# Kernel optimization log

Measured on AMD Instinct MI355X. Metric: run time of the kernel, lower is better.

## Reference

```python
import jax, jax.numpy as jnp
import numpy as np

IMAGE_SIZE = 1280
STRIDES = (8, 16, 32)
NUM_CLASSES = 80
BPC = 3  # boxes per cell
NMS_THRESH = 0.5
CONF_THRESH = 0.3
K_LEVEL = 1000
K_TOTAL = 3 * K_LEVEL
CLASS_OFFSET = 1.0e7  # shift boxes per class so cross-class IoU == 0 (== per-class NMS)
ANCHORS = np.array([[10,13],[16,30],[33,23],[30,61],[62,45],[59,119],
                    [116,90],[156,198],[373,326]], np.float32).reshape(3, 3, 2)

def level_anchors(level):
    f = IMAGE_SIZE // STRIDES[level]
    gy, gx = jnp.meshgrid(jnp.arange(f), jnp.arange(f), indexing='ij')
    xy = jnp.stack([gx, gy], -1).astype(jnp.float32).reshape(f * f, 1, 2)
    xy = jnp.broadcast_to(xy, (f * f, BPC, 2)).reshape(-1, 2)
    wh = jnp.broadcast_to(jnp.asarray(ANCHORS[level]), (f * f, BPC, 2)).reshape(-1, 2)
    return jnp.concatenate([xy, wh], -1)  # [M, 4]

def decode_boxes(anchors, reg, level):
    ctr = (jax.nn.sigmoid(reg[:, :2]) + anchors[:, :2]) * STRIDES[level]
    wh = jnp.exp(reg[:, 2:]) * anchors[:, 2:]
    return jnp.concatenate([ctr - wh * 0.5, ctr + wh * 0.5], -1)  # [M, 4] x1y1x2y2

def topk_level(obj, cls, reg, level):
    boxes = decode_boxes(level_anchors(level), reg, level)          # [M, 4]
    scores = jnp.sqrt(jax.nn.sigmoid(obj) * jax.nn.sigmoid(cls))    # [M, C]
    top_s, top_i = jax.lax.top_k(scores.reshape(-1), K_LEVEL)       # over M*C
    anchor_idx = top_i // NUM_CLASSES
    labels = top_i % NUM_CLASSES
    return top_s, labels, boxes[anchor_idx]

def nms_keep(boxes, scores, labels, valid):
    # Replicate source nms(): decoded x1y1x2y2 boxes are (re-)treated as cxcywh.
    b = jnp.concatenate([boxes[:, :2] - boxes[:, 2:] * 0.5,
                         boxes[:, :2] + boxes[:, 2:] * 0.5], -1)
    # class-aware: offset x-coords per class label
    off = labels.astype(jnp.float32) * CLASS_OFFSET
    b = b + off[:, None] * jnp.array([1.0, 0.0, 1.0, 0.0], b.dtype)
    x1, y1, x2, y2 = b[:, 0], b[:, 1], b[:, 2], b[:, 3]
    area = (x2 - x1) * (y2 - y1)
    xx1 = jnp.maximum(x1[:, None], x1[None, :])
    yy1 = jnp.maximum(y1[:, None], y1[None, :])
    xx2 = jnp.minimum(x2[:, None], x2[None, :])
    yy2 = jnp.minimum(y2[:, None], y2[None, :])
    inter = jnp.maximum(1e-10, xx2 - xx1) * jnp.maximum(1e-10, yy2 - yy1)
    iou = inter / (area[:, None] + area[None, :] - inter + 1e-14)   # [K, K]
    idx = jnp.arange(boxes.shape[0])
    def body(i, keep):
        sup = (iou[i] > NMS_THRESH) & (idx > i) & keep[i]
        return keep & ~sup
    return jax.lax.fori_loop(0, boxes.shape[0], body, valid)

def setup_inputs():
    key = jax.random.key(0)
    ks = jax.random.split(key, 9)
    d = {}
    for lvl, M in enumerate([76800, 19200, 4800]):
        d[f'obj{lvl}'] = jax.random.normal(ks[3 * lvl + 0], (M, 1), jnp.float32)
        d[f'cls{lvl}'] = jax.random.normal(ks[3 * lvl + 1], (M, NUM_CLASSES), jnp.float32)
        d[f'reg{lvl}'] = jax.random.normal(ks[3 * lvl + 2], (M, 4), jnp.float32)
    return d

def reference(obj0, cls0, reg0, obj1, cls1, reg1, obj2, cls2, reg2):
    levels = [(obj0, cls0, reg0), (obj1, cls1, reg1), (obj2, cls2, reg2)]
    ss, ls, bs = zip(*[topk_level(o, c, r, lvl) for lvl, (o, c, r) in enumerate(levels)])
    scores = jnp.concatenate(ss)        # [K_TOTAL]
    labels = jnp.concatenate(ls)
    boxes = jnp.concatenate(bs)         # [K_TOTAL, 4]
    # global sort by score (descending) so greedy NMS visits in score order
    scores, order = jax.lax.top_k(scores, K_TOTAL)
    labels = labels[order]
    boxes = boxes[order]
    valid = scores > CONF_THRESH
    keep = nms_keep(boxes, scores, labels, valid)
    out_boxes = jnp.where(keep[:, None], boxes, 0.0)
    out_scores = jnp.where(keep, scores, 0.0)
    out_labels = jnp.where(keep, labels, -1).astype(jnp.int32)
    return out_boxes, out_scores, out_labels, keep
```

## Files before the change

kernel.cpp:

```cpp
#include <hip/hip_runtime.h>
#include <hip/hip_bf16.h>
#include <math.h>

typedef unsigned int u32;
typedef unsigned long long u64;

#define NCLS 80
#define KLVL 1000
#define CAP  8192
#define TARGET_S 160u

#define OFF_CAND   0u
#define OFF_HIST   196608u
#define OFF_CNT    221184u
#define OFF_GFLAT  221216u
#define OFF_GSB    233216u
#define OFF_QX1    245216u
#define OFF_QY1    257216u
#define OFF_QX2    269216u
#define OFF_QY2    281216u
#define OFF_AREA   293216u
#define OFF_SCORE  305216u
#define OFF_LABEL  317216u
#define OFF_VALID  329216u
#define OFF_OBOX   341216u

__constant__ float cANCH[3][3][2] = {
  {{10.f,13.f},{16.f,30.f},{33.f,23.f}},
  {{30.f,61.f},{62.f,45.f},{59.f,119.f}},
  {{116.f,90.f},{156.f,198.f},{373.f,326.f}}
};

__device__ __forceinline__ float sig_fast(float x) {
  return 1.0f / (1.0f + __expf(-x));
}
__device__ __forceinline__ float sig_crit(float x) {
#pragma clang fp contract(off)
  double e = exp(-(double)x);
  float ef = (float)e;
  return 1.0f / (1.0f + ef);
}

__global__ __launch_bounds__(256) void kA(u32* __restrict__ hist,
                                          u32* __restrict__ cnt,
                                          u32* __restrict__ gsbits,
                                          u32* __restrict__ gflat) {
  int t = blockIdx.x * 256 + threadIdx.x;
  if (t < 6144) hist[t] = 0u;
  else if (t < 6152) cnt[t - 6144] = 0u;
  else if (t < 9152) gsbits[t - 6152] = 0u;
  else if (t < 12152) gflat[t - 9152] = 0u;
}

__global__ __launch_bounds__(256) void kB_s(const float* __restrict__ c0,
                                            const float* __restrict__ c1,
                                            const float* __restrict__ c2,
                                            const float* __restrict__ o0,
                                            const float* __restrict__ o1,
                                            const float* __restrict__ o2,
                                            u32* __restrict__ ghist) {
  __shared__ u32 lh[2048];
  for (int i = threadIdx.x; i < 2048; i += 256) lh[i] = 0u;
  __syncthreads();
  int bid = blockIdx.x;
  int l, e0; const float* cls; const float* obj;
  if (bid < 375)      { l = 0; e0 = (bid * 16 + 8) * 1024;         cls = c0; obj = o0; }
  else if (bid < 469) { l = 1; e0 = ((bid - 375) * 16 + 8) * 1024; cls = c1; obj = o1; }
  else                { l = 2; e0 = ((bid - 469) * 16 + 8) * 1024; cls = c2; obj = o2; }
  int e = e0 + threadIdx.x * 4;
  float4 cv = *(const float4*)(cls + e);
  float so = sig_fast(obj[e / 80]);
  float cc[4] = {cv.x, cv.y, cv.z, cv.w};
#pragma unroll
  for (int k = 0; k < 4; k++) {
    float p = so * sig_fast(cc[k]);
    atomicAdd(&lh[__float_as_uint(p) >> 19], 1u);
  }
  __syncthreads();
  for (int i = threadIdx.x; i < 2048; i += 256) {
    u32 v = lh[i];
    if (v) atomicAdd(&ghist[l * 2048 + i], v);
  }
}

__global__ __launch_bounds__(64) void k2(const u32* __restrict__ ghist,
                                         u32* __restrict__ cnt) {
  int l = blockIdx.x;
  int lane = threadIdx.x;
  const u32* h = ghist + l * 2048;
  int top = 2047 - lane * 32;
  u32 s = 0;
#pragma unroll
  for (int i = 0; i < 32; i++) s += h[top - i];
  u32 pre = s;
#pragma unroll
  for (int off = 1; off < 64; off <<= 1) {
    u32 o = __shfl_up(pre, off);
    if (lane >= off) pre += o;
  }
  u64 m = __ballot(pre >= TARGET_S);
  if (m == 0ull) { if (lane == 0) cnt[4 + l] = 0u; return; }
  int sel = __ffsll((long long)m) - 1;
  if (lane == sel) {
    u32 c = pre - s;
    u32 bb = 0u;
    for (int i = 0; i < 32; i++) {
      c += h[top - i];
      if (c >= TARGET_S) { bb = (u32)(top - i); break; }
    }
    cnt[4 + l] = bb << 19;
  }
}

__device__ __forceinline__ void block_map(int bid, int& l, int& e0) {
  if (bid < 6000)      { l = 0; e0 = bid * 1024; }
  else if (bid < 7500) { l = 1; e0 = (bid - 6000) * 1024; }
  else                 { l = 2; e0 = (bid - 7500) * 1024; }
}

__global__ __launch_bounds__(256) void k3(const float* __restrict__ c0,
                                          const float* __restrict__ c1,
                                          const float* __restrict__ c2,
                                          const float* __restrict__ o0,
                                          const float* __restrict__ o1,
                                          const float* __restrict__ o2,
                                          u32* __restrict__ cnt,
                                          u64* __restrict__ cand) {
  int l, e0; block_map(blockIdx.x, l, e0);
  const float* cls = (l == 0) ? c0 : (l == 1) ? c1 : c2;
  const float* obj = (l == 0) ? o0 : (l == 1) ? o1 : o2;
  u32 T = cnt[4 + l];
  u32 Tm = (T > 64u) ? (T - 64u) : 0u;
  int e = e0 + threadIdx.x * 4;
  float4 cv = *(const float4*)(cls + e);
  int a = e / 80;
  float so = sig_fast(obj[a]);
  float cc[4] = {cv.x, cv.y, cv.z, cv.w};
#pragma unroll
  for (int k = 0; k < 4; k++) {
    float pch = so * sig_fast(cc[k]);
    if (__float_as_uint(pch) >= Tm) {
      float soe = sig_crit(obj[a]);
      float sce = sig_crit(cc[k]);
      float p = soe * sce;
      u32 bits = __float_as_uint(p);
      if (bits >= T) {
        u32 slot = atomicAdd(&cnt[l], 1u);
        if (slot < CAP) {
          float s = __fsqrt_rn(p);
          u64 key = ((u64)__float_as_uint(s) << 32) | (u32)(~((u32)(e + k)));
          cand[(size_t)l * CAP + slot] = key;
        }
      }
    }
  }
}

__global__ __launch_bounds__(64) void r1(const u64* __restrict__ cand,
                                         const u32* __restrict__ cnt,
                                         u32* __restrict__ gsbits,
                                         u32* __restrict__ gflat) {
  __shared__ u64 S[CAP];
  int l = blockIdx.x >> 7;
  int b = blockIdx.x & 127;
  u32 n = cnt[l]; if (n > CAP) n = CAP;
  if ((u32)(b * 64) >= n) return;
  const u64* base = cand + (size_t)l * CAP;
  for (u32 i = threadIdx.x; i < n; i += 64) S[i] = base[i];
  __syncthreads();
  u32 idx = (u32)(b * 64 + threadIdx.x);
  u64 my = (idx < n) ? S[idx] : 0ull;
  u32 rank = 0;
#pragma unroll 8
  for (u32 i = 0; i < n; ++i) rank += (S[i] > my) ? 1u : 0u;
  if (idx < n && rank < KLVL) {
    gsbits[l * KLVL + rank] = (u32)(my >> 32);
    gflat [l * KLVL + rank] = ~((u32)my);
  }
}

__global__ __launch_bounds__(64) void rk6(const float* __restrict__ r0,
                                          const float* __restrict__ r1_,
                                          const float* __restrict__ r2_,
                                          const u32* __restrict__ gsbits,
                                          const u32* __restrict__ gflat,
                                          float* __restrict__ qx1, float* __restrict__ qy1,
                                          float* __restrict__ qx2, float* __restrict__ qy2,
                                          float* __restrict__ area,
                                          float* __restrict__ score,
                                          u32* __restrict__ label,
                                          u32* __restrict__ valid,
                                          float* __restrict__ obox,
                                          float* __restrict__ out) {
#pragma clang fp contract(off)
  __shared__ u32 SB[3000];
  int t = blockIdx.x * 64 + threadIdx.x;
  for (u32 i = threadIdx.x; i < 3000; i += 64) SB[i] = gsbits[i];
  __syncthreads();
  if (t >= 3000) return;
  ((float4*)out)[t] = make_float4(0.f, 0.f, 0.f, 0.f);
  out[12000 + t] = 0.0f;
  out[15000 + t] = -1.0f;
  out[18000 + t] = 0.0f;
  u32 myb = SB[t];
  u64 my = (((u64)myb) << 32) | (u32)(~t);
  u32 rank = 0;
#pragma unroll 8
  for (int i = 0; i < 3000; ++i) {
    u64 k = (((u64)SB[i]) << 32) | (u32)(~i);
    rank += (k > my) ? 1u : 0u;
  }
  int l = t / 1000;
  u32 flat = gflat[t];
  float sc = __uint_as_float(myb);
  int a = (int)(flat / NCLS), c = (int)(flat % NCLS);
  int cell = a / 3, bi = a % 3;
  int f = (l == 0) ? 160 : (l == 1) ? 80 : 40;
  float stride = (float)(8 << l);
  float gx = (float)(cell % f), gy = (float)(cell / f);
  const float* rp = ((l == 0) ? r0 : (l == 1) ? r1_ : r2_) + (size_t)a * 4;
  float t0 = rp[0], t1 = rp[1], t2 = rp[2], t3 = rp[3];
  float sx = 1.0f / (1.0f + expf(-t0));
  float sy = 1.0f / (1.0f + expf(-t1));
  float w = expf(t2) * cANCH[l][bi][0];
  float h = expf(t3) * cANCH[l][bi][1];
  float cx = (sx + gx) * stride;
  float cy = (sy + gy) * stride;
  float hw = w * 0.5f, hh = h * 0.5f;
  float x1 = cx - hw, y1 = cy - hh, x2 = cx + hw, y2 = cy + hh;
  ((float4*)obox)[rank] = make_float4(x1, y1, x2, y2);
  float hx2 = x2 * 0.5f, hy2 = y2 * 0.5f;
  float bx1 = x1 - hx2, by1 = y1 - hy2, bx2 = x1 + hx2, by2 = y1 + hy2;
  float off = (float)c * 1e7f;
  float a1 = bx1 + off, a2 = bx2 + off;
  qx1[rank] = a1; qy1[rank] = by1; qx2[rank] = a2; qy2[rank] = by2;
  area[rank] = (a2 - a1) * (by2 - by1);
  score[rank] = sc; label[rank] = (u32)c;
  valid[rank] = (sc > 0.3f) ? 1u : 0u;
}

#define CAPC 1024
__global__ __launch_bounds__(64) void k7(const float* __restrict__ qx1,
                                         const float* __restrict__ qy1,
                                         const float* __restrict__ qx2,
                                         const float* __restrict__ qy2,
                                         const float* __restrict__ area,
                                         const float* __restrict__ score,
                                         const u32* __restrict__ label,
                                         const u32* __restrict__ valid,
                                         const float* __restrict__ obox,
                                         float* __restrict__ out) {
#pragma clang fp contract(off)
  __shared__ u32 LIST[CAPC];
  __shared__ float X1[CAPC], Y1[CAPC], X2[CAPC], Y2[CAPC], AR[CAPC];
  __shared__ u32 KP[CAPC];
  u32 c = blockIdx.x;
  int lane = threadIdx.x;
  u32 n = 0;
  for (int base = 0; base < 3000; base += 64) {
    int j = base + lane;
    bool m = false;
    if (j < 3000) m = (label[j] == c) && (valid[j] != 0u);
    u64 mask = __ballot(m ? 1 : 0);
    u32 pos = n + (u32)__popcll(mask & ((1ull << lane) - 1ull));
    if (m && pos < CAPC) {
      LIST[pos] = (u32)j;
      X1[pos] = qx1[j]; Y1[pos] = qy1[j];
      X2[pos] = qx2[j]; Y2[pos] = qy2[j];
      AR[pos] = area[j]; KP[pos] = 1u;
    }
    n += (u32)__popcll(mask);
  }
  if (n > CAPC) n = CAPC;
  __syncthreads();
  for (u32 i = 0; i < n; ++i) {
    if (KP[i]) {
      float xi1 = X1[i], yi1 = Y1[i], xi2 = X2[i], yi2 = Y2[i], ai = AR[i];
      for (u32 j = i + 1 + (u32)lane; j < n; j += 64) {
        if (KP[j]) {
          float xx1 = fmaxf(xi1, X1[j]);
          float yy1 = fmaxf(yi1, Y1[j]);
          float xx2 = fminf(xi2, X2[j]);
          float yy2 = fminf(yi2, Y2[j]);
          float iw = xx2 - xx1, ih = yy2 - yy1;
          float inter = fmaxf(1e-10f, iw) * fmaxf(1e-10f, ih);
          float den = ai + AR[j] - inter + 1e-14f;
          if (inter / den > 0.5f) KP[j] = 0u;
        }
      }
    }
    __syncthreads();
  }
  for (u32 j = (u32)lane; j < n; j += 64) {
    if (KP[j]) {
      u32 r = LIST[j];
      float4 bx = ((const float4*)obox)[r];
      ((float4*)out)[r] = bx;
      out[12000 + r] = score[r];
      out[15000 + r] = (float)(int)c;
      out[18000 + r] = 1.0f;
    }
  }
}

extern "C" void kernel_launch(void* const* d_in, const int* in_sizes, int n_in,
                              void* d_out, int out_size, void* d_ws, size_t ws_size,
                              hipStream_t stream) {
  const float* obj0 = (const float*)d_in[0];
  const float* cls0 = (const float*)d_in[1];
  const float* reg0 = (const float*)d_in[2];
  const float* obj1 = (const float*)d_in[3];
  const float* cls1 = (const float*)d_in[4];
  const float* reg1 = (const float*)d_in[5];
  const float* obj2 = (const float*)d_in[6];
  const float* cls2 = (const float*)d_in[7];
  const float* reg2 = (const float*)d_in[8];
  char* ws = (char*)d_ws;
  u64* cand   = (u64*)(ws + OFF_CAND);
  u32* hist   = (u32*)(ws + OFF_HIST);
  u32* cnt    = (u32*)(ws + OFF_CNT);
  u32* gflat  = (u32*)(ws + OFF_GFLAT);
  u32* gsbits = (u32*)(ws + OFF_GSB);
  float* qx1  = (float*)(ws + OFF_QX1);
  float* qy1  = (float*)(ws + OFF_QY1);
  float* qx2  = (float*)(ws + OFF_QX2);
  float* qy2  = (float*)(ws + OFF_QY2);
  float* area = (float*)(ws + OFF_AREA);
  float* score= (float*)(ws + OFF_SCORE);
  u32* label  = (u32*)(ws + OFF_LABEL);
  u32* valid  = (u32*)(ws + OFF_VALID);
  float* obox = (float*)(ws + OFF_OBOX);
  float* out  = (float*)d_out;

  kA<<<48, 256, 0, stream>>>(hist, cnt, gsbits, gflat);
  kB_s<<<492, 256, 0, stream>>>(cls0, cls1, cls2, obj0, obj1, obj2, hist);
  k2<<<3, 64, 0, stream>>>(hist, cnt);
  k3<<<7875, 256, 0, stream>>>(cls0, cls1, cls2, obj0, obj1, obj2, cnt, cand);
  r1<<<384, 64, 0, stream>>>(cand, cnt, gsbits, gflat);
  rk6<<<47, 64, 0, stream>>>(reg0, reg1, reg2, gsbits, gflat,
                             qx1, qy1, qx2, qy2, area, score, label, valid, obox, out);
  k7<<<80, 64, 0, stream>>>(qx1, qy1, qx2, qy2, area, score, label, valid, obox, out);
}
```

Baseline: 332.1 us.

## Precompute per-anchor logit thresholds and filter 16-class chunks by max

Adds a small kernel that converts each anchor's objectness and the level threshold into a minimum class logit, so the candidate scan can reject classes by a raw compare instead of evaluating a sigmoid per element. The candidate kernel becomes grid-stride, loads 16 floats per thread, and skips a whole chunk when its max is below the per-anchor bound. The cost is an extra launch and a small cmin buffer. Correctness relies on the margins in the inverse-sigmoid bound being conservative.

```diff
diff --git a/kernel.cpp b/kernel.cpp
--- a/kernel.cpp
+++ b/kernel.cpp
@@ -24,6 +24,7 @@
 #define OFF_LABEL  317216u
 #define OFF_VALID  329216u
 #define OFF_OBOX   341216u
+#define OFF_CMIN   389216u
 
 __constant__ float cANCH[3][3][2] = {
   {{10.f,13.f},{16.f,30.f},{33.f,23.f}},
@@ -112,10 +113,35 @@
   }
 }
 
-__device__ __forceinline__ void block_map(int bid, int& l, int& e0) {
-  if (bid < 6000)      { l = 0; e0 = bid * 1024; }
-  else if (bid < 7500) { l = 1; e0 = (bid - 6000) * 1024; }
-  else                 { l = 2; e0 = (bid - 7500) * 1024; }
+__global__ __launch_bounds__(256) void kO(const float* __restrict__ o0,
+                                          const float* __restrict__ o1,
+                                          const float* __restrict__ o2,
+                                          const u32* __restrict__ cnt,
+                                          float* __restrict__ cmin) {
+  int t = blockIdx.x * 256 + threadIdx.x;
+  if (t >= 100800) return;
+  const float* o; int a; int l;
+  if (t < 76800)      { o = o0; a = t;         l = 0; }
+  else if (t < 96000) { o = o1; a = t - 76800; l = 1; }
+  else                { o = o2; a = t - 96000; l = 2; }
+  float tthr = __uint_as_float(cnt[4 + l]);
+  float so = sig_fast(o[a]);
+  float so_hi = so * (1.0f + 8e-6f);
+  float c_min;
+  if (so_hi < tthr) {
+    c_min = __int_as_float(0x7f800000);
+  } else {
+    float u_lo = (tthr / so_hi) * (1.0f - 4e-6f);
+    c_min = __logf(u_lo) - __logf(1.0f - u_lo) - 1e-3f;
+  }
+  cmin[t] = c_min;
+}
+
+__device__ __forceinline__ void k3_map(int bid, int& l, int& b0, int& nb,
+                                       int& nch, int& ab) {
+  if (bid < 512)      { l = 0; b0 = 0;   nb = 512; nch = 384000; ab = 0; }
+  else if (bid < 704) { l = 1; b0 = 512; nb = 192; nch = 96000;  ab = 76800; }
+  else                { l = 2; b0 = 704; nb = 64;  nch = 24000;  ab = 96000; }
 }
 
 __global__ __launch_bounds__(256) void k3(const float* __restrict__ c0,
@@ -124,32 +150,45 @@
                                           const float* __restrict__ o0,
                                           const float* __restrict__ o1,
                                           const float* __restrict__ o2,
+                                          const float* __restrict__ cmin,
                                           u32* __restrict__ cnt,
                                           u64* __restrict__ cand) {
-  int l, e0; block_map(blockIdx.x, l, e0);
+  int l, b0, nb, nch, ab;
+  k3_map(blockIdx.x, l, b0, nb, nch, ab);
   const float* cls = (l == 0) ? c0 : (l == 1) ? c1 : c2;
   const float* obj = (l == 0) ? o0 : (l == 1) ? o1 : o2;
   u32 T = cnt[4 + l];
-  u32 Tm = (T > 64u) ? (T - 64u) : 0u;
-  int e = e0 + threadIdx.x * 4;
-  float4 cv = *(const float4*)(cls + e);
-  int a = e / 80;
-  float so = sig_fast(obj[a]);
-  float cc[4] = {cv.x, cv.y, cv.z, cv.w};
+  int tid = (blockIdx.x - b0) * 256 + (int)threadIdx.x;
+  int nth = nb * 256;
+  for (int ch = tid; ch < nch; ch += nth) {
+    int e = ch * 16;
+    int a = ch / 5;
+    float cm = cmin[ab + a];
+    const float4* p4 = (const float4*)(cls + e);
+    float4 v0 = p4[0], v1 = p4[1], v2 = p4[2], v3 = p4[3];
+    float m0 = fmaxf(fmaxf(v0.x, v0.y), fmaxf(v0.z, v0.w));
+    float m1 = fmaxf(fmaxf(v1.x, v1.y), fmaxf(v1.z, v1.w));
+    float m2 = fmaxf(fmaxf(v2.x, v2.y), fmaxf(v2.z, v2.w));
+    float m3 = fmaxf(fmaxf(v3.x, v3.y), fmaxf(v3.z, v3.w));
+    float m = fmaxf(fmaxf(m0, m1), fmaxf(m2, m3));
+    if (m >= cm) {
+      float soe = sig_crit(obj[a]);
+      float cc[16] = {v0.x, v0.y, v0.z, v0.w, v1.x, v1.y, v1.z, v1.w,
+                      v2.x, v2.y, v2.z, v2.w, v3.x, v3.y, v3.z, v3.w};
 #pragma unroll
-  for (int k = 0; k < 4; k++) {
-    float pch = so * sig_fast(cc[k]);
-    if (__float_as_uint(pch) >= Tm) {
-      float soe = sig_crit(obj[a]);
-      float sce = sig_crit(cc[k]);
-      float p = soe * sce;
-      u32 bits = __float_as_uint(p);
-      if (bits >= T) {
-        u32 slot = atomicAdd(&cnt[l], 1u);
-        if (slot < CAP) {
-          float s = __fsqrt_rn(p);
-          u64 key = ((u64)__float_as_uint(s) << 32) | (u32)(~((u32)(e + k)));
-          cand[(size_t)l * CAP + slot] = key;
+      for (int k = 0; k < 16; k++) {
+        if (cc[k] >= cm) {
+          float sce = sig_crit(cc[k]);
+          float p = soe * sce;
+          u32 bits = __float_as_uint(p);
+          if (bits >= T) {
+            u32 slot = atomicAdd(&cnt[l], 1u);
+            if (slot < CAP) {
+              float s = __fsqrt_rn(p);
+              u64 key = ((u64)__float_as_uint(s) << 32) | (u32)(~((u32)(e + k)));
+              cand[(size_t)l * CAP + slot] = key;
+            }
+          }
         }
       }
     }
@@ -330,12 +369,14 @@
   u32* label  = (u32*)(ws + OFF_LABEL);
   u32* valid  = (u32*)(ws + OFF_VALID);
   float* obox = (float*)(ws + OFF_OBOX);
+  float* cmin = (float*)(ws + OFF_CMIN);
   float* out  = (float*)d_out;
 
   kA<<<48, 256, 0, stream>>>(hist, cnt, gsbits, gflat);
   kB_s<<<492, 256, 0, stream>>>(cls0, cls1, cls2, obj0, obj1, obj2, hist);
   k2<<<3, 64, 0, stream>>>(hist, cnt);
-  k3<<<7875, 256, 0, stream>>>(cls0, cls1, cls2, obj0, obj1, obj2, cnt, cand);
+  kO<<<394, 256, 0, stream>>>(obj0, obj1, obj2, cnt, cmin);
+  k3<<<768, 256, 0, stream>>>(cls0, cls1, cls2, obj0, obj1, obj2, cmin, cnt, cand);
   r1<<<384, 64, 0, stream>>>(cand, cnt, gsbits, gflat);
   rk6<<<47, 64, 0, stream>>>(reg0, reg1, reg2, gsbits, gflat,
                              qx1, qy1, qx2, qy2, area, score, label, valid, obox, out);
```

New measurement: 356.8 us. 1.07x slower.

## Precompute per-anchor logit cutoff and filter class logits without sigmoid

Applied to the files above, without the earlier changes.

Fuses the threshold-finding kernel with a new per-anchor pass that inverts the sigmoid product threshold into a minimum class logit per anchor. The candidate-extraction kernel then compares raw class logits (max of each float4) against this cutoff, skipping per-element sigmoid evaluation, and runs as a grid-stride loop with eight float4 loads in flight per thread. This removes transcendental work and the fixed large grid from the bandwidth-bound scan. It relies on the safety margins in the inverted cutoff being conservative enough not to drop candidates near the threshold.

```diff
diff --git a/kernel.cpp b/kernel.cpp
--- a/kernel.cpp
+++ b/kernel.cpp
@@ -9,6 +9,11 @@
 #define KLVL 1000
 #define CAP  8192
 #define TARGET_S 160u
+
+#define TC 2016000u
+#define C1 1536000u
+#define C2 1920000u
+#define INFF __int_as_float(0x7f800000)
 
 #define OFF_CAND   0u
 #define OFF_HIST   196608u
@@ -24,6 +29,7 @@
 #define OFF_LABEL  317216u
 #define OFF_VALID  329216u
 #define OFF_OBOX   341216u
+#define OFF_CMIN   389216u
 
 __constant__ float cANCH[3][3][2] = {
   {{10.f,13.f},{16.f,30.f},{33.f,23.f}},
@@ -83,64 +89,85 @@
   }
 }
 
-__global__ __launch_bounds__(64) void k2(const u32* __restrict__ ghist,
-                                         u32* __restrict__ cnt) {
-  int l = blockIdx.x;
-  int lane = threadIdx.x;
-  const u32* h = ghist + l * 2048;
-  int top = 2047 - lane * 32;
-  u32 s = 0;
+__global__ __launch_bounds__(256) void kO2(const float* __restrict__ o0,
+                                           const float* __restrict__ o1,
+                                           const float* __restrict__ o2,
+                                           const u32* __restrict__ ghist,
+                                           u32* __restrict__ cnt,
+                                           float* __restrict__ cmin) {
+  __shared__ u32 s_tbits;
+  int blk = blockIdx.x;
+  int t0 = blk * 256;
+  int l = (t0 < 76800) ? 0 : (t0 < 96000) ? 1 : 2;
+  if (threadIdx.x < 64) {
+    int lane = threadIdx.x;
+    const u32* h = ghist + l * 2048;
+    int top = 2047 - lane * 32;
+    u32 s = 0;
 #pragma unroll
-  for (int i = 0; i < 32; i++) s += h[top - i];
-  u32 pre = s;
+    for (int i = 0; i < 32; i++) s += h[top - i];
+    u32 pre = s;
 #pragma unroll
-  for (int off = 1; off < 64; off <<= 1) {
-    u32 o = __shfl_up(pre, off);
-    if (lane >= off) pre += o;
-  }
-  u64 m = __ballot(pre >= TARGET_S);
-  if (m == 0ull) { if (lane == 0) cnt[4 + l] = 0u; return; }
-  int sel = __ffsll((long long)m) - 1;
-  if (lane == sel) {
-    u32 c = pre - s;
-    u32 bb = 0u;
-    for (int i = 0; i < 32; i++) {
-      c += h[top - i];
-      if (c >= TARGET_S) { bb = (u32)(top - i); break; }
-    }
-    cnt[4 + l] = bb << 19;
-  }
-}
-
-__device__ __forceinline__ void block_map(int bid, int& l, int& e0) {
-  if (bid < 6000)      { l = 0; e0 = bid * 1024; }
-  else if (bid < 7500) { l = 1; e0 = (bid - 6000) * 1024; }
-  else                 { l = 2; e0 = (bid - 7500) * 1024; }
-}
-
-__global__ __launch_bounds__(256) void k3(const float* __restrict__ c0,
-                                          const float* __restrict__ c1,
-                                          const float* __restrict__ c2,
+    for (int off = 1; off < 64; off <<= 1) {
+      u32 o = __shfl_up(pre, off);
+      if (lane >= off) pre += o;
+    }
+    u64 m = __ballot(pre >= TARGET_S);
+    if (m == 0ull) { if (lane == 0) s_tbits = 0u; }
+    else {
+      int sel = __ffsll((long long)m) - 1;
+      if (lane == sel) {
+        u32 c = pre - s;
+        u32 bb = 0u;
+        for (int i = 0; i < 32; i++) {
+          c += h[top - i];
+          if (c >= TARGET_S) { bb = (u32)(top - i); break; }
+        }
+        s_tbits = bb << 19;
+      }
+    }
+  }
+  __syncthreads();
+  u32 tbits = s_tbits;
+  if (threadIdx.x == 0 && (blk == 0 || blk == 300 || blk == 375))
+    cnt[4 + l] = tbits;
+  int t = t0 + (int)threadIdx.x;
+  if (t >= 100800) return;
+  const float* o; int a;
+  if (t < 76800)      { o = o0; a = t; }
+  else if (t < 96000) { o = o1; a = t - 76800; }
+  else                { o = o2; a = t - 96000; }
+  float tthr = __uint_as_float(tbits);
+  float so = sig_fast(o[a]);
+  float so_hi = so * (1.0f + 8e-6f);
+  float c_min;
+  if (so_hi < tthr) {
+    c_min = INFF;
+  } else {
+    float u_lo = (tthr / so_hi) * (1.0f - 4e-6f);
+    c_min = __logf(u_lo) - __logf(1.0f - u_lo) - 1e-3f;
+  }
+  cmin[t] = c_min;
+}
+
+__device__ __forceinline__ void slow_path(u32 c, float4 v, float cm,
                                           const float* __restrict__ o0,
                                           const float* __restrict__ o1,
                                           const float* __restrict__ o2,
                                           u32* __restrict__ cnt,
                                           u64* __restrict__ cand) {
-  int l, e0; block_map(blockIdx.x, l, e0);
-  const float* cls = (l == 0) ? c0 : (l == 1) ? c1 : c2;
-  const float* obj = (l == 0) ? o0 : (l == 1) ? o1 : o2;
+  int l; u32 base, abase; const float* obj;
+  if (c < C1)      { l = 0; base = 0;  abase = 0;      obj = o0; }
+  else if (c < C2) { l = 1; base = C1; abase = 76800u; obj = o1; }
+  else             { l = 2; base = C2; abase = 96000u; obj = o2; }
+  u32 a_loc = c / 20u - abase;
+  u32 e_loc = (c - base) * 4u;
+  float soe = sig_crit(obj[a_loc]);
   u32 T = cnt[4 + l];
-  u32 Tm = (T > 64u) ? (T - 64u) : 0u;
-  int e = e0 + threadIdx.x * 4;
-  float4 cv = *(const float4*)(cls + e);
-  int a = e / 80;
-  float so = sig_fast(obj[a]);
-  float cc[4] = {cv.x, cv.y, cv.z, cv.w};
+  float cc[4] = {v.x, v.y, v.z, v.w};
 #pragma unroll
   for (int k = 0; k < 4; k++) {
-    float pch = so * sig_fast(cc[k]);
-    if (__float_as_uint(pch) >= Tm) {
-      float soe = sig_crit(obj[a]);
+    if (cc[k] >= cm) {
       float sce = sig_crit(cc[k]);
       float p = soe * sce;
       u32 bits = __float_as_uint(p);
@@ -148,11 +175,48 @@
         u32 slot = atomicAdd(&cnt[l], 1u);
         if (slot < CAP) {
           float s = __fsqrt_rn(p);
-          u64 key = ((u64)__float_as_uint(s) << 32) | (u32)(~((u32)(e + k)));
+          u64 key = ((u64)__float_as_uint(s) << 32) | (u32)(~(e_loc + (u32)k));
           cand[(size_t)l * CAP + slot] = key;
         }
       }
     }
+  }
+}
+
+#define K3_LOAD(J)                                                         \
+  u32 c##J = cbase + (J) * 256u + tid;                                     \
+  float4 v##J = make_float4(0.f, 0.f, 0.f, 0.f);                           \
+  float cm##J = INFF;                                                      \
+  if (c##J < TC) {                                                         \
+    const float* p;                                                        \
+    if (c##J < C1)      p = cls0 + (size_t)c##J * 4u;                      \
+    else if (c##J < C2) p = cls1 + (size_t)(c##J - C1) * 4u;               \
+    else                p = cls2 + (size_t)(c##J - C2) * 4u;               \
+    v##J = *(const float4*)p;                                              \
+    cm##J = cmin[c##J / 20u];                                              \
+  }
+
+#define K3_PROC(J) {                                                       \
+    float m = fmaxf(fmaxf(v##J.x, v##J.y), fmaxf(v##J.z, v##J.w));         \
+    if (m >= cm##J) slow_path(c##J, v##J, cm##J, o0, o1, o2, cnt, cand);   \
+  }
+
+__global__ __launch_bounds__(256) void k3(const float* __restrict__ cls0,
+                                          const float* __restrict__ cls1,
+                                          const float* __restrict__ cls2,
+                                          const float* __restrict__ o0,
+                                          const float* __restrict__ o1,
+                                          const float* __restrict__ o2,
+                                          const float* __restrict__ cmin,
+                                          u32* __restrict__ cnt,
+                                          u64* __restrict__ cand) {
+  u32 tid = threadIdx.x;
+  for (u32 cbase = (u32)blockIdx.x * 2048u; cbase < TC;
+       cbase += (u32)gridDim.x * 2048u) {
+    K3_LOAD(0) K3_LOAD(1) K3_LOAD(2) K3_LOAD(3)
+    K3_LOAD(4) K3_LOAD(5) K3_LOAD(6) K3_LOAD(7)
+    K3_PROC(0) K3_PROC(1) K3_PROC(2) K3_PROC(3)
+    K3_PROC(4) K3_PROC(5) K3_PROC(6) K3_PROC(7)
   }
 }
 
@@ -330,12 +394,13 @@
   u32* label  = (u32*)(ws + OFF_LABEL);
   u32* valid  = (u32*)(ws + OFF_VALID);
   float* obox = (float*)(ws + OFF_OBOX);
+  float* cmin = (float*)(ws + OFF_CMIN);
   float* out  = (float*)d_out;
 
   kA<<<48, 256, 0, stream>>>(hist, cnt, gsbits, gflat);
   kB_s<<<492, 256, 0, stream>>>(cls0, cls1, cls2, obj0, obj1, obj2, hist);
-  k2<<<3, 64, 0, stream>>>(hist, cnt);
-  k3<<<7875, 256, 0, stream>>>(cls0, cls1, cls2, obj0, obj1, obj2, cnt, cand);
+  kO2<<<394, 256, 0, stream>>>(obj0, obj1, obj2, hist, cnt, cmin);
+  k3<<<960, 256, 0, stream>>>(cls0, cls1, cls2, obj0, obj1, obj2, cmin, cnt, cand);
   r1<<<384, 64, 0, stream>>>(cand, cnt, gsbits, gflat);
   rk6<<<47, 64, 0, stream>>>(reg0, reg1, reg2, gsbits, gflat,
                              qx1, qy1, qx2, qy2, area, score, label, valid, obox, out);
```

Result: slower. 477.1 us (+43.7%).
